# Kernel optimization log

Measured on AMD Instinct MI355X. Metric: run time of the kernel, lower is better.

## Reference

```python
import jax, jax.numpy as jnp
import numpy as np

DIM_X, H1, H2 = 1024, 2048, 512
SL, SU = 8192, 16384
K_TRIES = 8  # vectorized stand-in for the per-sample rejection-sampling while-loop


def setup_inputs() -> dict:
    key = jax.random.key(0)
    ks = jax.random.split(key, 10)
    s = 0.02
    return {
        "X_l": jax.random.normal(ks[0], (SL, DIM_X), jnp.float32),
        "y_l": jax.random.normal(ks[1], (SL,), jnp.float32),
        "X_u": jax.random.normal(ks[2], (SU, DIM_X), jnp.float32),
        "y_u": jax.random.normal(ks[3], (SU,), jnp.float32),
        "W1": jax.random.normal(ks[4], (DIM_X, H1), jnp.float32) * s,
        "b1": jnp.zeros((H1,), jnp.float32),
        "W2": jax.random.normal(ks[5], (H1, H2), jnp.float32) * s,
        "b2": jnp.zeros((H2,), jnp.float32),
        "W3": jax.random.normal(ks[6], (H2, 1), jnp.float32) * s,
        "b3": jnp.zeros((1,), jnp.float32),
    }


def _sample_pairs(key, y_l, size_u):
    """For each unlabeled sample, draw a labeled pair (a, b) with a != b and
    y_l[a] != y_l[b] (mirrors torch.randperm + rejection loop). K candidate
    draws per sample; first valid candidate is taken (valid w.h.p. for
    continuous y_l)."""
    size_l = y_l.shape[0]
    ka, kb = jax.random.split(key)
    ia = jax.random.randint(ka, (size_u, K_TRIES), 0, size_l)  # [SU, K]
    ib = jax.random.randint(kb, (size_u, K_TRIES), 0, size_l)
    valid = (ia != ib) & (y_l[ia] != y_l[ib])
    first = jnp.argmax(valid, axis=1)  # first valid candidate per row
    a = jnp.take_along_axis(ia, first[:, None], axis=1)[:, 0]
    b = jnp.take_along_axis(ib, first[:, None], axis=1)[:, 0]
    return a, b


def reference(X_l, y_l, X_u, y_u, W1, b1, W2, b2, W3, b3):
    def encode(x):
        h = jax.nn.relu(x @ W1 + b1)
        return jax.nn.relu(h @ W2 + b2)

    feat_l = encode(X_l)          # [SL, H2]
    feat_u = encode(X_u)          # [SU, H2]
    y_hat = feat_l @ W3 + b3      # [SL, 1]

    a, b = _sample_pairs(jax.random.key(42), y_l, X_u.shape[0])
    k = (y_u - y_l[b]) / (y_l[a] - y_l[b])            # [SU]
    feat_comb = k[:, None] * feat_l[a] + (1.0 - k)[:, None] * feat_l[b]
    return feat_u, feat_comb, y_hat
```

## Files before the change

### kernel.cpp

```cpp
#include <hip/hip_runtime.h>
#include <stdint.h>

#define SLAB 8192
#define SUNL 16384
#define DIMX 1024
#define HID1 2048
#define HID2 512
#define KTRIES 8
#define MTOT (SLAB + SUNL)

typedef __attribute__((ext_vector_type(8))) short bf16x8;
typedef __attribute__((ext_vector_type(4))) float f32x4;

__device__ __forceinline__ unsigned short f2bf(float f) {
  union { float f; uint32_t u; } c; c.f = f;
  return (unsigned short)((c.u + 0x7fffu + ((c.u >> 16) & 1u)) >> 16);
}

__device__ __forceinline__ void async16(const void* g, void* l) {
  __builtin_amdgcn_global_load_lds(
      (const __attribute__((address_space(1))) unsigned int*)g,
      (__attribute__((address_space(3))) unsigned int*)l,
      16, 0, 0);
}

struct U2 { uint32_t x, y; };

__device__ __forceinline__ U2 threefry(uint32_t k0, uint32_t k1, uint32_t x0, uint32_t x1) {
  uint32_t ks2 = k0 ^ k1 ^ 0x1BD11BDAu;
  x0 += k0; x1 += k1;
#define TF_R(r) { x0 += x1; x1 = (x1 << (r)) | (x1 >> (32 - (r))); x1 ^= x0; }
  TF_R(13) TF_R(15) TF_R(26) TF_R(6)
  x0 += k1; x1 += ks2 + 1u;
  TF_R(17) TF_R(29) TF_R(16) TF_R(24)
  x0 += ks2; x1 += k0 + 2u;
  TF_R(13) TF_R(15) TF_R(26) TF_R(6)
  x0 += k0; x1 += k1 + 3u;
  TF_R(17) TF_R(29) TF_R(16) TF_R(24)
  x0 += k1; x1 += ks2 + 4u;
  TF_R(13) TF_R(15) TF_R(26) TF_R(6)
  x0 += ks2; x1 += k0 + 5u;
#undef TF_R
  return {x0, x1};
}

#define XL_BLOCKS (SLAB * DIMX / 4 / 256)
#define CAST_BLOCKS (MTOT * DIMX / 4 / 256)
#define T1_NBX (HID1 / 32)
#define T1_BLOCKS ((HID1 / 32) * (DIMX / 32))
#define T2_NBX (HID2 / 32)
#define T2_BLOCKS ((HID2 / 32) * (HID1 / 32))
#define PAIR_BLOCKS (SUNL / 256)
#define PREP_BLOCKS (CAST_BLOCKS + T1_BLOCKS + T2_BLOCKS + PAIR_BLOCKS)

__global__ __launch_bounds__(256) void prep_kernel(
    const float* __restrict__ Xl, const float* __restrict__ Xu,
    const float* __restrict__ W1, const float* __restrict__ W2,
    const float* __restrict__ y_l, const float* __restrict__ y_u,
    unsigned short* __restrict__ X_bf, unsigned short* __restrict__ W1T,
    unsigned short* __restrict__ W2T,
    int* __restrict__ ia, int* __restrict__ ib, float* __restrict__ kv)
{
  __shared__ float t[32][33];
  int b = blockIdx.x;
  int tid = threadIdx.x;

  if (b < CAST_BLOCKS) {
    const float* src; size_t i, doff;
    if (b < XL_BLOCKS) { src = Xl; i = (size_t)b * 256 + tid; doff = 0; }
    else { src = Xu; i = (size_t)(b - XL_BLOCKS) * 256 + tid; doff = (size_t)SLAB * DIMX / 4; }
    float4 v = ((const float4*)src)[i];
    ushort4 o;
    o.x = f2bf(v.x); o.y = f2bf(v.y); o.z = f2bf(v.z); o.w = f2bf(v.w);
    ((ushort4*)X_bf)[doff + i] = o;
  } else if (b < CAST_BLOCKS + T1_BLOCKS + T2_BLOCKS) {
    const float* W; unsigned short* WT; int K, N, bx, by;
    if (b < CAST_BLOCKS + T1_BLOCKS) {
      int tb = b - CAST_BLOCKS;
      W = W1; WT = W1T; K = DIMX; N = HID1; bx = tb % T1_NBX; by = tb / T1_NBX;
    } else {
      int tb = b - CAST_BLOCKS - T1_BLOCKS;
      W = W2; WT = W2T; K = HID1; N = HID2; bx = tb % T2_NBX; by = tb / T2_NBX;
    }
    int k0 = by * 32, n0 = bx * 32;
    int tx = tid & 31, ty = tid >> 5;
#pragma unroll
    for (int i = 0; i < 32; i += 8)
      t[ty + i][tx] = W[(size_t)(k0 + ty + i) * N + n0 + tx];
    __syncthreads();
#pragma unroll
    for (int i = 0; i < 32; i += 8)
      WT[(size_t)(n0 + ty + i) * K + k0 + tx] = f2bf(t[tx][ty + i]);
  } else {
    int r = (b - CAST_BLOCKS - T1_BLOCKS - T2_BLOCKS) * 256 + tid;
    U2 ka  = threefry(0u, 42u, 0u, 0u);
    U2 kb  = threefry(0u, 42u, 0u, 1u);
    U2 k2a = threefry(ka.x, ka.y, 0u, 1u);
    U2 k2b = threefry(kb.x, kb.y, 0u, 1u);
    int iav[KTRIES], ibv[KTRIES];
#pragma unroll
    for (int c = 0; c < KTRIES; ++c) {
      uint32_t tt = (uint32_t)(r * KTRIES + c);
      U2 oa = threefry(k2a.x, k2a.y, 0u, tt);
      U2 ob = threefry(k2b.x, k2b.y, 0u, tt);
      iav[c] = (int)((oa.x ^ oa.y) & (SLAB - 1));
      ibv[c] = (int)((ob.x ^ ob.y) & (SLAB - 1));
    }
    int a = iav[0], bb2 = ibv[0];
#pragma unroll
    for (int c = 0; c < KTRIES; ++c) {
      if (iav[c] != ibv[c] && y_l[iav[c]] != y_l[ibv[c]]) { a = iav[c]; bb2 = ibv[c]; break; }
    }
    float ya = y_l[a], yb = y_l[bb2];
    ia[r] = a; ib[r] = bb2; kv[r] = (y_u[r] - yb) / (ya - yb);
  }
}

#define GROUP_M 8

template<int OUT_BF16, int RELU>
__global__ __launch_bounds__(256, 2) void gemm_bt_mfma(
    const unsigned short* __restrict__ A,
    const unsigned short* __restrict__ Bt,
    const float* __restrict__ bias,
    void* __restrict__ C0, void* __restrict__ C1, int Msplit,
    int M, int N, int K)
{
  __shared__ unsigned short As[256 * 32];
  __shared__ unsigned short Bs[128 * 32];

  const int tid  = threadIdx.x;
  const int wave = tid >> 6;
  const int lane = tid & 63;

  const int nbx = N / 128;
  const int gsize = nbx * GROUP_M;
  const int grp = blockIdx.x / gsize, within = blockIdx.x % gsize;
  const int m0 = (grp * GROUP_M + (within % GROUP_M)) * 256;
  const int n0 = (within / GROUP_M) * 128;

  const int wm = (wave >> 1) * 128;
  const int wn = (wave & 1) * 64;

  const int lrow = lane >> 2;
  const int srowA = wave * 64 + lrow;
  const int srowB = wave * 32 + lrow;
  const int gcA = ((lane & 3) - (srowA >> 1)) & 3;
  const int gcB = ((lane & 3) - (srowB >> 1)) & 3;
  const unsigned short* gA = A  + (size_t)(m0 + srowA) * K + gcA * 8;
  const unsigned short* gB = Bt + (size_t)(n0 + srowB) * K + gcB * 8;
  unsigned short* lA = As + wave * 64 * 32;
  unsigned short* lB = Bs + wave * 32 * 32;

  const int fr = lane & 15;
  const int q  = lane >> 4;

  f32x4 acc[8][4] = {};

  for (int k0 = 0; k0 < K; k0 += 32) {
#pragma unroll
    for (int c = 0; c < 4; ++c)
      async16(gA + k0 + (size_t)(c * 16) * K, lA + c * 16 * 32);
#pragma unroll
    for (int c = 0; c < 2; ++c)
      async16(gB + k0 + (size_t)(c * 16) * K, lB + c * 16 * 32);
    __syncthreads();

    bf16x8 ar[8], br[4];
#pragma unroll
    for (int i = 0; i < 8; ++i) {
      int rowA = wm + i * 16 + fr;
      ar[i] = *(const bf16x8*)(As + rowA * 32 + ((q + (rowA >> 1)) & 3) * 8);
    }
#pragma unroll
    for (int j = 0; j < 4; ++j) {
      int rowB = wn + j * 16 + fr;
      br[j] = *(const bf16x8*)(Bs + rowB * 32 + ((q + (rowB >> 1)) & 3) * 8);
    }
#pragma unroll
    for (int i = 0; i < 8; ++i)
#pragma unroll
      for (int j = 0; j < 4; ++j)
        acc[i][j] = __builtin_amdgcn_mfma_f32_16x16x32_bf16(ar[i], br[j], acc[i][j], 0, 0, 0);
    __syncthreads();
  }

  void* Cb = (m0 < Msplit) ? C0 : C1;
  const int mbase = (m0 < Msplit) ? m0 : (m0 - Msplit);
  const int crow = mbase + wm + (lane >> 4) * 4;
  const int ccol = n0 + wn + (lane & 15);
#pragma unroll
  for (int j = 0; j < 4; ++j) {
    float bv = bias[ccol + j * 16];
#pragma unroll
    for (int i = 0; i < 8; ++i) {
#pragma unroll
      for (int r = 0; r < 4; ++r) {
        float v = acc[i][j][r] + bv;
        if (RELU) v = fmaxf(v, 0.0f);
        size_t idx = (size_t)(crow + i * 16 + r) * N + ccol + j * 16;
        if (OUT_BF16) ((unsigned short*)Cb)[idx] = f2bf(v);
        else          ((float*)Cb)[idx] = v;
      }
    }
  }
}

#define COMB_BLOCKS (SUNL / 2)
#define YHAT_BLOCKS (SLAB / 4)
#define POST_BLOCKS (COMB_BLOCKS + YHAT_BLOCKS)

__global__ __launch_bounds__(256) void post_kernel(
    const float* __restrict__ feat_l, const float* __restrict__ W3,
    const float* __restrict__ b3, const int* __restrict__ ia,
    const int* __restrict__ ib, const float* __restrict__ kv,
    float* __restrict__ out_comb, float* __restrict__ out_yhat)
{
  int b = blockIdx.x;
  if (b < COMB_BLOCKS) {
    int row = b * 2 + (threadIdx.x >> 7);
    int c = (threadIdx.x & 127) << 2;
    float k = kv[row];
    float km1 = 1.0f - k;
    float4 fa = *(const float4*)(feat_l + (size_t)ia[row] * HID2 + c);
    float4 fb = *(const float4*)(feat_l + (size_t)ib[row] * HID2 + c);
    float4 o;
    o.x = k * fa.x + km1 * fb.x;
    o.y = k * fa.y + km1 * fb.y;
    o.z = k * fa.z + km1 * fb.z;
    o.w = k * fa.w + km1 * fb.w;
    *(float4*)(out_comb + (size_t)row * HID2 + c) = o;
  } else {
    int wave = threadIdx.x >> 6;
    int lane = threadIdx.x & 63;
    int row = (b - COMB_BLOCKS) * 4 + wave;
    const float* f = feat_l + (size_t)row * HID2;
    float s = 0.f;
#pragma unroll
    for (int j = 0; j < HID2 / 64; ++j) s = fmaf(f[lane + j * 64], W3[lane + j * 64], s);
#pragma unroll
    for (int off = 32; off; off >>= 1) s += __shfl_down(s, off);
    if (lane == 0) out_yhat[row] = s + b3[0];
  }
}

extern "C" void kernel_launch(void* const* d_in, const int* in_sizes, int n_in,
                              void* d_out, int out_size, void* d_ws, size_t ws_size,
                              hipStream_t stream)
{
  const float* X_l = (const float*)d_in[0];
  const float* y_l = (const float*)d_in[1];
  const float* X_u = (const float*)d_in[2];
  const float* y_u = (const float*)d_in[3];
  const float* W1  = (const float*)d_in[4];
  const float* b1  = (const float*)d_in[5];
  const float* W2  = (const float*)d_in[6];
  const float* b2  = (const float*)d_in[7];
  const float* W3  = (const float*)d_in[8];
  const float* b3  = (const float*)d_in[9];

  float* out_featu = (float*)d_out;
  float* out_comb  = out_featu + (size_t)SUNL * HID2;
  float* out_yhat  = out_comb + (size_t)SUNL * HID2;

  unsigned short* X_bf  = (unsigned short*)d_ws;
  unsigned short* W1T   = X_bf + (size_t)MTOT * DIMX;
  unsigned short* W2T   = W1T + (size_t)HID1 * DIMX;
  unsigned short* H_bf  = W2T + (size_t)HID2 * HID1;
  float* feat_l = (float*)(H_bf + (size_t)MTOT * HID1);
  int*   ai = (int*)(feat_l + (size_t)SLAB * HID2);
  int*   bi = ai + SUNL;
  float* kv = (float*)(bi + SUNL);

  dim3 blk(256);

  prep_kernel<<<dim3(PREP_BLOCKS), blk, 0, stream>>>(
      X_l, X_u, W1, W2, y_l, y_u, X_bf, W1T, W2T, ai, bi, kv);

  gemm_bt_mfma<1, 1><<<dim3((HID1 / 128) * (MTOT / 256)), blk, 0, stream>>>(
      X_bf, W1T, b1, H_bf, H_bf, MTOT * 2 , MTOT, HID1, DIMX);

  gemm_bt_mfma<0, 1><<<dim3((HID2 / 128) * (MTOT / 256)), blk, 0, stream>>>(
      H_bf, W2T, b2, feat_l, out_featu, SLAB, MTOT, HID2, HID1);

  post_kernel<<<dim3(POST_BLOCKS), blk, 0, stream>>>(
      feat_l, W3, b3, ai, bi, kv, out_comb, out_yhat);
}
```

Before: 373.0 us.

## Rewrite GEMM as 256x256-tile, 8-wave, double-buffered pipelined MFMA kernel

Replaces the single-buffered 256x128 GEMM with a 256x256 tile computed by 512 threads. K-steps are now 64 wide and the LDS buffers are double-buffered with async global-to-LDS loads. Each K-tile is split into four MFMA phases, with prefetch issue interleaved between them and explicit waitcnt, barriers and setprio to overlap memory with compute. An XOR swizzle on the LDS layout avoids bank conflicts. This targets load latency and LDS traffic per FLOP, at the cost of larger LDS use (128KB), lower occupancy, and fragile hand-tuned synchronisation.

```diff
diff --git a/kernel.cpp b/kernel.cpp
--- a/kernel.cpp
+++ b/kernel.cpp
@@ -117,72 +117,192 @@
 }
 
 #define GROUP_M 8
+#define MFMA_B16(a, b, c) __builtin_amdgcn_mfma_f32_16x16x32_bf16(a, b, c, 0, 0, 0)
+
+template<bool S1, bool S2, int VMC>
+__device__ __forceinline__ void ktile256(
+    unsigned short* Ac, unsigned short* Bc, unsigned short* Ao,
+    const unsigned short* gA, const unsigned short* gB,
+    int K, int k1, int k2, int ldst,
+    int abase, int bbase, int sw0, int sw1,
+    f32x4 (&acc)[8][4])
+{
+  bf16x8 a0[4][2], a1[4][2], b0[2][2], b1[2][2];
+
+#pragma unroll
+  for (int i = 0; i < 4; ++i) {
+    a0[i][0] = *(const bf16x8*)(Ac + abase + i * 1024 + sw0);
+    a0[i][1] = *(const bf16x8*)(Ac + abase + i * 1024 + sw1);
+  }
+#pragma unroll
+  for (int j = 0; j < 2; ++j) {
+    b0[j][0] = *(const bf16x8*)(Bc + bbase + j * 1024 + sw0);
+    b0[j][1] = *(const bf16x8*)(Bc + bbase + j * 1024 + sw1);
+  }
+  if (S1) {
+    async16(gA + (size_t)64 * K + k1,  Ao + 4096 + ldst);
+    async16(gA + (size_t)192 * K + k1, Ao + 12288 + ldst);
+  }
+  asm volatile("s_waitcnt lgkmcnt(8)");
+  __builtin_amdgcn_s_barrier();
+  asm volatile("s_waitcnt lgkmcnt(0)" ::: "memory");
+  __builtin_amdgcn_sched_barrier(0);
+  __builtin_amdgcn_s_setprio(1);
+#pragma unroll
+  for (int i = 0; i < 4; ++i)
+#pragma unroll
+    for (int j = 0; j < 2; ++j) {
+      acc[i][j] = MFMA_B16(a0[i][0], b0[j][0], acc[i][j]);
+      acc[i][j] = MFMA_B16(a0[i][1], b0[j][1], acc[i][j]);
+    }
+  __builtin_amdgcn_s_setprio(0);
+  __builtin_amdgcn_s_barrier();
+
+#pragma unroll
+  for (int j = 0; j < 2; ++j) {
+    b1[j][0] = *(const bf16x8*)(Bc + bbase + (j + 2) * 1024 + sw0);
+    b1[j][1] = *(const bf16x8*)(Bc + bbase + (j + 2) * 1024 + sw1);
+  }
+  if (S2) {
+    async16(gA + k2,                   Ac + ldst);
+    async16(gA + (size_t)128 * K + k2, Ac + 8192 + ldst);
+  }
+  __builtin_amdgcn_s_barrier();
+  asm volatile("s_waitcnt lgkmcnt(0)" ::: "memory");
+  __builtin_amdgcn_sched_barrier(0);
+  __builtin_amdgcn_s_setprio(1);
+#pragma unroll
+  for (int i = 0; i < 4; ++i)
+#pragma unroll
+    for (int j = 0; j < 2; ++j) {
+      acc[i][j + 2] = MFMA_B16(a0[i][0], b1[j][0], acc[i][j + 2]);
+      acc[i][j + 2] = MFMA_B16(a0[i][1], b1[j][1], acc[i][j + 2]);
+    }
+  __builtin_amdgcn_s_setprio(0);
+  __builtin_amdgcn_s_barrier();
+
+#pragma unroll
+  for (int i = 0; i < 4; ++i) {
+    a1[i][0] = *(const bf16x8*)(Ac + abase + (i + 4) * 1024 + sw0);
+    a1[i][1] = *(const bf16x8*)(Ac + abase + (i + 4) * 1024 + sw1);
+  }
+  if (S2) {
+    async16(gB + k2,                  Bc + ldst);
+    async16(gB + (size_t)64 * K + k2, Bc + 4096 + ldst);
+  }
+  __builtin_amdgcn_s_barrier();
+  asm volatile("s_waitcnt lgkmcnt(0)" ::: "memory");
+  __builtin_amdgcn_sched_barrier(0);
+  __builtin_amdgcn_s_setprio(1);
+#pragma unroll
+  for (int i = 0; i < 4; ++i)
+#pragma unroll
+    for (int j = 0; j < 2; ++j) {
+      acc[i + 4][j] = MFMA_B16(a1[i][0], b0[j][0], acc[i + 4][j]);
+      acc[i + 4][j] = MFMA_B16(a1[i][1], b0[j][1], acc[i + 4][j]);
+    }
+  __builtin_amdgcn_s_setprio(0);
+  __builtin_amdgcn_s_barrier();
+
+  if (S2) {
+    async16(gB + (size_t)128 * K + k2, Bc + 8192 + ldst);
+    async16(gB + (size_t)192 * K + k2, Bc + 12288 + ldst);
+  }
+  __builtin_amdgcn_s_barrier();
+  asm volatile("s_waitcnt lgkmcnt(0)" ::: "memory");
+  __builtin_amdgcn_sched_barrier(0);
+  __builtin_amdgcn_s_setprio(1);
+#pragma unroll
+  for (int i = 0; i < 4; ++i)
+#pragma unroll
+    for (int j = 0; j < 2; ++j) {
+      acc[i + 4][j + 2] = MFMA_B16(a1[i][0], b1[j][0], acc[i + 4][j + 2]);
+      acc[i + 4][j + 2] = MFMA_B16(a1[i][1], b1[j][1], acc[i + 4][j + 2]);
+    }
+  __builtin_amdgcn_s_setprio(0);
+  if (VMC == 6)      asm volatile("s_waitcnt vmcnt(6)" ::: "memory");
+  else if (VMC == 0) asm volatile("s_waitcnt vmcnt(0)" ::: "memory");
+  __builtin_amdgcn_s_barrier();
+}
 
 template<int OUT_BF16, int RELU>
-__global__ __launch_bounds__(256, 2) void gemm_bt_mfma(
+__global__ __launch_bounds__(512, 2) void gemm_bt_256(
     const unsigned short* __restrict__ A,
     const unsigned short* __restrict__ Bt,
     const float* __restrict__ bias,
     void* __restrict__ C0, void* __restrict__ C1, int Msplit,
     int M, int N, int K)
 {
-  __shared__ unsigned short As[256 * 32];
-  __shared__ unsigned short Bs[128 * 32];
+  __shared__ unsigned short As[2][16384];
+  __shared__ unsigned short Bs[2][16384];
 
   const int tid  = threadIdx.x;
   const int wave = tid >> 6;
   const int lane = tid & 63;
 
-  const int nbx = N / 128;
+  const int nbx = N >> 8;
   const int gsize = nbx * GROUP_M;
   const int grp = blockIdx.x / gsize, within = blockIdx.x % gsize;
-  const int m0 = (grp * GROUP_M + (within % GROUP_M)) * 256;
-  const int n0 = (within / GROUP_M) * 128;
-
-  const int wm = (wave >> 1) * 128;
-  const int wn = (wave & 1) * 64;
-
-  const int lrow = lane >> 2;
-  const int srowA = wave * 64 + lrow;
-  const int srowB = wave * 32 + lrow;
-  const int gcA = ((lane & 3) - (srowA >> 1)) & 3;
-  const int gcB = ((lane & 3) - (srowB >> 1)) & 3;
-  const unsigned short* gA = A  + (size_t)(m0 + srowA) * K + gcA * 8;
-  const unsigned short* gB = Bt + (size_t)(n0 + srowB) * K + gcB * 8;
-  unsigned short* lA = As + wave * 64 * 32;
-  unsigned short* lB = Bs + wave * 32 * 32;
-
-  const int fr = lane & 15;
-  const int q  = lane >> 4;
+  const int m0 = (grp * GROUP_M + (within % GROUP_M)) << 8;
+  const int n0 = (within / GROUP_M) << 8;
+
+  const int wm = (wave >> 2) << 7;
+  const int wn = (wave & 3) << 6;
+
+  const int srow   = tid >> 3;
+  const int schunk = (tid & 7) ^ (srow & 7);
+  const unsigned short* gA = A  + (size_t)(m0 + srow) * K + schunk * 8;
+  const unsigned short* gB = Bt + (size_t)(n0 + srow) * K + schunk * 8;
+  const int ldst = wave << 9;
+
+  const int fr = lane & 15, q = lane >> 4;
+  const int sw0 = (q << 3) ^ ((fr & 7) << 3);
+  const int sw1 = sw0 ^ 32;
+  const int abase = (wm + fr) << 6;
+  const int bbase = (wn + fr) << 6;
 
   f32x4 acc[8][4] = {};
 
-  for (int k0 = 0; k0 < K; k0 += 32) {
-#pragma unroll
-    for (int c = 0; c < 4; ++c)
-      async16(gA + k0 + (size_t)(c * 16) * K, lA + c * 16 * 32);
-#pragma unroll
-    for (int c = 0; c < 2; ++c)
-      async16(gB + k0 + (size_t)(c * 16) * K, lB + c * 16 * 32);
-    __syncthreads();
-
-    bf16x8 ar[8], br[4];
-#pragma unroll
-    for (int i = 0; i < 8; ++i) {
-      int rowA = wm + i * 16 + fr;
-      ar[i] = *(const bf16x8*)(As + rowA * 32 + ((q + (rowA >> 1)) & 3) * 8);
-    }
-#pragma unroll
-    for (int j = 0; j < 4; ++j) {
-      int rowB = wn + j * 16 + fr;
-      br[j] = *(const bf16x8*)(Bs + rowB * 32 + ((q + (rowB >> 1)) & 3) * 8);
-    }
-#pragma unroll
-    for (int i = 0; i < 8; ++i)
-#pragma unroll
-      for (int j = 0; j < 4; ++j)
-        acc[i][j] = __builtin_amdgcn_mfma_f32_16x16x32_bf16(ar[i], br[j], acc[i][j], 0, 0, 0);
-    __syncthreads();
+  unsigned short* A0p = &As[0][0]; unsigned short* B0p = &Bs[0][0];
+  unsigned short* A1p = &As[1][0]; unsigned short* B1p = &Bs[1][0];
+
+  async16(gA,                        A0p + ldst);
+  async16(gA + (size_t)64 * K,       A0p + 4096 + ldst);
+  async16(gA + (size_t)128 * K,      A0p + 8192 + ldst);
+  async16(gA + (size_t)192 * K,      A0p + 12288 + ldst);
+  async16(gB,                        B0p + ldst);
+  async16(gB + (size_t)64 * K,       B0p + 4096 + ldst);
+  async16(gB + (size_t)128 * K,      B0p + 8192 + ldst);
+  async16(gB + (size_t)192 * K,      B0p + 12288 + ldst);
+  asm volatile("s_waitcnt vmcnt(4)" ::: "memory");
+  async16(gA + 64,                   A1p + ldst);
+  async16(gA + (size_t)128 * K + 64, A1p + 8192 + ldst);
+  async16(gB + 64,                   B1p + ldst);
+  async16(gB + (size_t)64 * K + 64,  B1p + 4096 + ldst);
+  async16(gB + (size_t)128 * K + 64, B1p + 8192 + ldst);
+  async16(gB + (size_t)192 * K + 64, B1p + 12288 + ldst);
+  asm volatile("s_waitcnt vmcnt(6)" ::: "memory");
+  __builtin_amdgcn_s_barrier();
+
+  const int NT = K >> 6;
+#pragma unroll 1
+  for (int t = 0; t < NT - 2; ++t) {
+    const int bb = t & 1;
+    ktile256<true, true, 6>(&As[bb][0], &Bs[bb][0], &As[bb ^ 1][0],
+                            gA, gB, K, (t + 1) << 6, (t + 2) << 6,
+                            ldst, abase, bbase, sw0, sw1, acc);
+  }
+  {
+    const int bb = (NT - 2) & 1;
+    ktile256<true, false, 0>(&As[bb][0], &Bs[bb][0], &As[bb ^ 1][0],
+                             gA, gB, K, (NT - 1) << 6, 0,
+                             ldst, abase, bbase, sw0, sw1, acc);
+  }
+  {
+    const int bb = (NT - 1) & 1;
+    ktile256<false, false, -1>(&As[bb][0], &Bs[bb][0], &As[bb ^ 1][0],
+                               gA, gB, K, 0, 0,
+                               ldst, abase, bbase, sw0, sw1, acc);
   }
 
   void* Cb = (m0 < Msplit) ? C0 : C1;
@@ -272,17 +392,15 @@
   int*   bi = ai + SUNL;
   float* kv = (float*)(bi + SUNL);
 
-  dim3 blk(256);
-
-  prep_kernel<<<dim3(PREP_BLOCKS), blk, 0, stream>>>(
+  prep_kernel<<<dim3(PREP_BLOCKS), dim3(256), 0, stream>>>(
       X_l, X_u, W1, W2, y_l, y_u, X_bf, W1T, W2T, ai, bi, kv);
 
-  gemm_bt_mfma<1, 1><<<dim3((HID1 / 128) * (MTOT / 256)), blk, 0, stream>>>(
-      X_bf, W1T, b1, H_bf, H_bf, MTOT * 2 , MTOT, HID1, DIMX);
-
-  gemm_bt_mfma<0, 1><<<dim3((HID2 / 128) * (MTOT / 256)), blk, 0, stream>>>(
+  gemm_bt_256<1, 1><<<dim3((HID1 / 256) * (MTOT / 256)), dim3(512), 0, stream>>>(
+      X_bf, W1T, b1, H_bf, H_bf, MTOT , MTOT, HID1, DIMX);
+
+  gemm_bt_256<0, 1><<<dim3((HID2 / 256) * (MTOT / 256)), dim3(512), 0, stream>>>(
       H_bf, W2T, b2, feat_l, out_featu, SLAB, MTOT, HID2, HID1);
 
-  post_kernel<<<dim3(POST_BLOCKS), blk, 0, stream>>>(
+  post_kernel<<<dim3(POST_BLOCKS), dim3(256), 0, stream>>>(
       feat_l, W3, b3, ai, bi, kv, out_comb, out_yhat);
 }
```

New measurement: 377.2 us. No clear change (+1.1%).
